# Kernel optimization log

Measured on AMD Instinct MI355X. Metric: run time of the kernel, lower is better.

Reference implementation:

```python
import jax, jax.numpy as jnp
import numpy as np

B, N, IN_DIM, OUT_DIM, K = 64, 256, 512, 512, 8
DK = OUT_DIM // K  # per-kernel feature dim


def setup_inputs() -> dict:
    key = jax.random.key(0)
    k1, k2, k3, k4 = jax.random.split(key, 4)
    node_feats = jax.random.normal(k1, (B, N, IN_DIM), dtype=jnp.float32)
    adj = jax.random.uniform(k2, (B, K, N, N), dtype=jnp.float32)
    weight = jax.random.normal(k3, (IN_DIM, OUT_DIM), dtype=jnp.float32) * (1.0 / np.sqrt(IN_DIM))
    bias = jax.random.normal(k4, (OUT_DIM,), dtype=jnp.float32) * 0.01
    return {"node_feats": node_feats, "adj": adj, "weight": weight, "bias": bias}


def reference(node_feats, adj, weight, bias):
    # kernel linear + ReLU: (b, n, out_dim)
    h = jax.nn.relu(jnp.einsum('bni,io->bno', node_feats, weight) + bias)
    # split into kernel slots: (b, n, k, dk)
    h = h.reshape(B, N, K, DK)
    # graph.aggregate: per-kernel dense message passing over adjacency
    # out[b,n,k,d] = sum_m adj[b,k,n,m] * h[b,m,k,d]
    agg = jnp.einsum('bknm,bmkd->bnkd', adj, h)
    return agg.reshape(B, N, OUT_DIM)
```

## Files before the change

kernel.cpp:

```cpp
#include <hip/hip_runtime.h>
#include <hip/hip_bf16.h>


typedef __attribute__((ext_vector_type(8))) short short8;
typedef __attribute__((ext_vector_type(4))) float floatx4;

__device__ __forceinline__ unsigned short f2bf(float f) {
    union { float f; unsigned u; } v; v.f = f;
    unsigned r = v.u + 0x7FFFu + ((v.u >> 16) & 1u);
    return (unsigned short)(r >> 16);
}

__device__ __forceinline__ unsigned pk2bf(float a, float b) {
    union { __hip_bfloat162 h; unsigned u; } cv;
    cv.h = __float22bfloat162_rn(make_float2(a, b));
    return cv.u;
}

__global__ __launch_bounds__(256) void wfrag_kernel(const float* __restrict__ W,
                                                    unsigned short* __restrict__ Wf) {
    __shared__ unsigned short t[32 * 66];
    const int blk = blockIdx.x;
    const int k0 = (blk & 15) * 32;
    const int o0 = (blk >> 4) * 64;
    const int tid = threadIdx.x;
#pragma unroll
    for (int j = 0; j < 8; ++j) {
        int idx = tid + j * 256;
        int oc = idx & 63, kr = idx >> 6;
        t[kr * 66 + oc] = f2bf(W[(size_t)(k0 + kr) * 512 + o0 + oc]);
    }
    __syncthreads();
#pragma unroll
    for (int j = 0; j < 8; ++j) {
        int idx = tid + j * 256;
        int kk = idx & 31, dr = idx >> 5;
        Wf[(size_t)blk * 2048 + dr * 32 + kk] = t[kk * 66 + dr];
    }
}

__global__ __launch_bounds__(256, 5) void lin_kernel(
    const float* __restrict__ X, const unsigned short* __restrict__ Wf,
    const float* __restrict__ bias, unsigned short* __restrict__ hF) {
    __shared__ unsigned short xt[2][128 * 40];

    const int W_ = (blockIdx.x & 7) * 128 + (blockIdx.x >> 3);
    const int mh = W_ & 1;
    const int ks = (W_ >> 1) & 7;
    const int b  = W_ >> 4;

    const int tid = threadIdx.x;
    const int lane = tid & 63, w = tid >> 6;
    const int lrow = lane & 15, quad = lane >> 4;

    const float* xsrc = X + (size_t)b * 131072
                          + (size_t)(mh * 128 + (tid >> 1)) * 512 + (tid & 1) * 16;
    const int xw = (tid >> 1) * 40 + (tid & 1) * 16;

    const unsigned short* wfp = Wf + (size_t)ks * 32768 + lrow * 32 + quad * 8;

    float bv[4];
#pragma unroll
    for (int dt = 0; dt < 4; ++dt) bv[dt] = bias[ks * 64 + dt * 16 + lrow];

    floatx4 acc[2][4];
    const floatx4 fzero = {0.f, 0.f, 0.f, 0.f};
#pragma unroll
    for (int g = 0; g < 2; ++g)
#pragma unroll
        for (int j = 0; j < 4; ++j) acc[g][j] = fzero;

    float4 r[4];
#define LLOAD(kb) do {                                                  \
        r[0] = *(const float4*)(xsrc + (kb) * 32);                      \
        r[1] = *(const float4*)(xsrc + (kb) * 32 + 4);                  \
        r[2] = *(const float4*)(xsrc + (kb) * 32 + 8);                  \
        r[3] = *(const float4*)(xsrc + (kb) * 32 + 12);                 \
    } while (0)
#define LWRITE(buf) do {                                                \
        union { short8 s; unsigned u[4]; } t0_, t1_;                    \
        t0_.u[0] = pk2bf(r[0].x, r[0].y); t0_.u[1] = pk2bf(r[0].z, r[0].w); \
        t0_.u[2] = pk2bf(r[1].x, r[1].y); t0_.u[3] = pk2bf(r[1].z, r[1].w); \
        t1_.u[0] = pk2bf(r[2].x, r[2].y); t1_.u[1] = pk2bf(r[2].z, r[2].w); \
        t1_.u[2] = pk2bf(r[3].x, r[3].y); t1_.u[3] = pk2bf(r[3].z, r[3].w); \
        *(short8*)(xt[buf] + xw) = t0_.s;                               \
        *(short8*)(xt[buf] + xw + 8) = t1_.s;                           \
    } while (0)

    LLOAD(0);
    LWRITE(0);
    LLOAD(1);
    __syncthreads();

#pragma unroll
    for (int kb = 0; kb < 16; ++kb) {
        const int buf = kb & 1;
        if (kb < 15) {
            LWRITE(buf ^ 1);
            if (kb < 14) LLOAD(kb + 2);
        }
        short8 a0 = *(const short8*)(xt[buf] + (w * 32 + lrow) * 40 + quad * 8);
        short8 a1 = *(const short8*)(xt[buf] + (w * 32 + 16 + lrow) * 40 + quad * 8);
#pragma unroll
        for (int dt = 0; dt < 4; ++dt) {
            short8 wfr = *(const short8*)(wfp + kb * 2048 + dt * 512);
            acc[0][dt] = __builtin_amdgcn_mfma_f32_16x16x32_bf16(a0, wfr, acc[0][dt], 0, 0, 0);
            acc[1][dt] = __builtin_amdgcn_mfma_f32_16x16x32_bf16(a1, wfr, acc[1][dt], 0, 0, 0);
        }
        if (kb < 15) __syncthreads();
    }
#undef LLOAD
#undef LWRITE

    unsigned short* hs = hF + (size_t)(b * 8 + ks) * 16384 + (size_t)(mh * 4 + w) * 2048;
#pragma unroll
    for (int g = 0; g < 2; ++g) {
#pragma unroll
        for (int dt = 0; dt < 4; ++dt) {
            floatx4 c = acc[g][dt];
            uint2 pv;
            pv.x = pk2bf(fmaxf(c.x + bv[dt], 0.f), fmaxf(c.y + bv[dt], 0.f));
            pv.y = pk2bf(fmaxf(c.z + bv[dt], 0.f), fmaxf(c.w + bv[dt], 0.f));
            *(uint2*)(hs + dt * 512 + lrow * 32 + g * 16 + quad * 4) = pv;
        }
    }
}

__global__ __launch_bounds__(256, 5) void agg_kernel(
    const unsigned short* __restrict__ hF, const float* __restrict__ adj,
    float* __restrict__ out) {
    __shared__ unsigned short at[2][128 * 40];

    const int W_ = (blockIdx.x & 7) * 128 + (blockIdx.x >> 3);
    const int nt = W_ & 1;
    const int ks = (W_ >> 1) & 7;
    const int b  = W_ >> 4;

    const int tid = threadIdx.x;
    const int lane = tid & 63, w = tid >> 6;
    const int lrow = lane & 15, quad = lane >> 4;

    const float* asrc = adj + (size_t)(b * 8 + ks) * 65536
                            + (size_t)(nt * 128 + (tid >> 1)) * 256 + (tid & 1) * 16;
    const int aw = (tid >> 1) * 40 + (tid & 1) * 16;

    const unsigned short* hfp = hF + (size_t)(b * 8 + ks) * 16384 + lrow * 32 + quad * 8;

    floatx4 acc[2][4];
    const floatx4 fzero = {0.f, 0.f, 0.f, 0.f};
#pragma unroll
    for (int g = 0; g < 2; ++g)
#pragma unroll
        for (int j = 0; j < 4; ++j) acc[g][j] = fzero;

    float4 r[4];
#define ALOAD(mt) do {                                                  \
        r[0] = *(const float4*)(asrc + (mt) * 32);                      \
        r[1] = *(const float4*)(asrc + (mt) * 32 + 4);                  \
        r[2] = *(const float4*)(asrc + (mt) * 32 + 8);                  \
        r[3] = *(const float4*)(asrc + (mt) * 32 + 12);                 \
    } while (0)
#define AWRITE(buf) do {                                                \
        union { short8 s; unsigned u[4]; } t0_, t1_;                    \
        t0_.u[0] = pk2bf(r[0].x, r[0].y); t0_.u[1] = pk2bf(r[0].z, r[0].w); \
        t0_.u[2] = pk2bf(r[1].x, r[1].y); t0_.u[3] = pk2bf(r[1].z, r[1].w); \
        t1_.u[0] = pk2bf(r[2].x, r[2].y); t1_.u[1] = pk2bf(r[2].z, r[2].w); \
        t1_.u[2] = pk2bf(r[3].x, r[3].y); t1_.u[3] = pk2bf(r[3].z, r[3].w); \
        *(short8*)(at[buf] + aw) = t0_.s;                               \
        *(short8*)(at[buf] + aw + 8) = t1_.s;                           \
    } while (0)

    ALOAD(0);
    AWRITE(0);
    ALOAD(1);
    __syncthreads();

#pragma unroll
    for (int mt = 0; mt < 8; ++mt) {
        const int buf = mt & 1;
        if (mt < 7) {
            AWRITE(buf ^ 1);
            if (mt < 6) ALOAD(mt + 2);
        }
        short8 a0 = *(const short8*)(at[buf] + (w * 32 + lrow) * 40 + quad * 8);
        short8 a1 = *(const short8*)(at[buf] + (w * 32 + 16 + lrow) * 40 + quad * 8);
#pragma unroll
        for (int dt = 0; dt < 4; ++dt) {
            short8 hfr = *(const short8*)(hfp + mt * 2048 + dt * 512);
            acc[0][dt] = __builtin_amdgcn_mfma_f32_16x16x32_bf16(a0, hfr, acc[0][dt], 0, 0, 0);
            acc[1][dt] = __builtin_amdgcn_mfma_f32_16x16x32_bf16(a1, hfr, acc[1][dt], 0, 0, 0);
        }
        if (mt < 7) __syncthreads();
    }
#undef ALOAD
#undef AWRITE

#pragma unroll
    for (int g = 0; g < 2; ++g) {
        const int n0 = nt * 128 + w * 32 + g * 16 + quad * 4;
        float* dst = out + ((size_t)b * 256 + n0) * 512 + ks * 64 + lrow;
#pragma unroll
        for (int dt = 0; dt < 4; ++dt) {
            float* p = dst + dt * 16;
            p[0 * 512] = acc[g][dt].x;
            p[1 * 512] = acc[g][dt].y;
            p[2 * 512] = acc[g][dt].z;
            p[3 * 512] = acc[g][dt].w;
        }
    }
}

extern "C" void kernel_launch(void* const* d_in, const int* in_sizes, int n_in,
                              void* d_out, int out_size, void* d_ws, size_t ws_size,
                              hipStream_t stream) {
    const float* X    = (const float*)d_in[0];
    const float* adj  = (const float*)d_in[1];
    const float* W    = (const float*)d_in[2];
    const float* bias = (const float*)d_in[3];
    float* out = (float*)d_out;

    unsigned short* Wf = (unsigned short*)d_ws;
    unsigned short* hF = Wf + 512 * 512;

    wfrag_kernel<<<128, 256, 0, stream>>>(W, Wf);
    lin_kernel<<<1024, 256, 0, stream>>>(X, Wf, bias, hF);
    agg_kernel<<<1024, 256, 0, stream>>>(hF, adj, out);
}
```

Before: 271.5 us.

## Single-buffer LDS with register double-buffered prefetch and lighter barriers

Both GEMM kernels drop the double-buffered LDS tile for a single buffer and keep two register sets of fp32 global loads, prefetching two tiles ahead. Weight and h fragments for the next step are also prefetched into registers. The __syncthreads calls become explicit lgkmcnt waits plus s_barrier wrapped in sched_barrier, and launch bounds drop from 5 to 4 waves per SIMD. This is meant to hide global-load latency better, at the cost of two barriers per iteration, higher register pressure and lower occupancy.

```diff
diff --git a/kernel.cpp b/kernel.cpp
--- a/kernel.cpp
+++ b/kernel.cpp
@@ -15,6 +15,13 @@
     union { __hip_bfloat162 h; unsigned u; } cv;
     cv.h = __float22bfloat162_rn(make_float2(a, b));
     return cv.u;
+}
+
+__device__ __forceinline__ void lds_barrier() {
+    __builtin_amdgcn_sched_barrier(0);
+    asm volatile("s_waitcnt lgkmcnt(0)" ::: "memory");
+    __builtin_amdgcn_s_barrier();
+    __builtin_amdgcn_sched_barrier(0);
 }
 
 __global__ __launch_bounds__(256) void wfrag_kernel(const float* __restrict__ W,
@@ -39,10 +46,10 @@
     }
 }
 
-__global__ __launch_bounds__(256, 5) void lin_kernel(
+__global__ __launch_bounds__(256, 4) void lin_kernel(
     const float* __restrict__ X, const unsigned short* __restrict__ Wf,
     const float* __restrict__ bias, unsigned short* __restrict__ hF) {
-    __shared__ unsigned short xt[2][128 * 40];
+    __shared__ unsigned short xt[128 * 40];
 
     const int W_ = (blockIdx.x & 7) * 128 + (blockIdx.x >> 3);
     const int mh = W_ & 1;
@@ -70,44 +77,50 @@
 #pragma unroll
         for (int j = 0; j < 4; ++j) acc[g][j] = fzero;
 
-    float4 r[4];
-#define LLOAD(kb) do {                                                  \
+    float4 ra[4], rb[4];
+    short8 wc[4], wn[4];
+
+#define LLOAD(r, kb) do {                                               \
         r[0] = *(const float4*)(xsrc + (kb) * 32);                      \
         r[1] = *(const float4*)(xsrc + (kb) * 32 + 4);                  \
         r[2] = *(const float4*)(xsrc + (kb) * 32 + 8);                  \
         r[3] = *(const float4*)(xsrc + (kb) * 32 + 12);                 \
     } while (0)
-#define LWRITE(buf) do {                                                \
+#define LWRITE(r) do {                                                  \
         union { short8 s; unsigned u[4]; } t0_, t1_;                    \
         t0_.u[0] = pk2bf(r[0].x, r[0].y); t0_.u[1] = pk2bf(r[0].z, r[0].w); \
         t0_.u[2] = pk2bf(r[1].x, r[1].y); t0_.u[3] = pk2bf(r[1].z, r[1].w); \
         t1_.u[0] = pk2bf(r[2].x, r[2].y); t1_.u[1] = pk2bf(r[2].z, r[2].w); \
         t1_.u[2] = pk2bf(r[3].x, r[3].y); t1_.u[3] = pk2bf(r[3].z, r[3].w); \
-        *(short8*)(xt[buf] + xw) = t0_.s;                               \
-        *(short8*)(xt[buf] + xw + 8) = t1_.s;                           \
-    } while (0)
-
-    LLOAD(0);
-    LWRITE(0);
-    LLOAD(1);
-    __syncthreads();
+        *(short8*)(xt + xw) = t0_.s;                                    \
+        *(short8*)(xt + xw + 8) = t1_.s;                                \
+    } while (0)
+
+    LLOAD(ra, 0);
+    LLOAD(rb, 1);
+#pragma unroll
+    for (int dt = 0; dt < 4; ++dt) wc[dt] = *(const short8*)(wfp + dt * 512);
 
 #pragma unroll
     for (int kb = 0; kb < 16; ++kb) {
-        const int buf = kb & 1;
+        if (kb > 0) lds_barrier();
+        if (kb & 1) { LWRITE(rb); if (kb < 14) LLOAD(rb, kb + 2); }
+        else        { LWRITE(ra); if (kb < 14) LLOAD(ra, kb + 2); }
         if (kb < 15) {
-            LWRITE(buf ^ 1);
-            if (kb < 14) LLOAD(kb + 2);
-        }
-        short8 a0 = *(const short8*)(xt[buf] + (w * 32 + lrow) * 40 + quad * 8);
-        short8 a1 = *(const short8*)(xt[buf] + (w * 32 + 16 + lrow) * 40 + quad * 8);
-#pragma unroll
-        for (int dt = 0; dt < 4; ++dt) {
-            short8 wfr = *(const short8*)(wfp + kb * 2048 + dt * 512);
-            acc[0][dt] = __builtin_amdgcn_mfma_f32_16x16x32_bf16(a0, wfr, acc[0][dt], 0, 0, 0);
-            acc[1][dt] = __builtin_amdgcn_mfma_f32_16x16x32_bf16(a1, wfr, acc[1][dt], 0, 0, 0);
-        }
-        if (kb < 15) __syncthreads();
+#pragma unroll
+            for (int dt = 0; dt < 4; ++dt)
+                wn[dt] = *(const short8*)(wfp + (kb + 1) * 2048 + dt * 512);
+        }
+        lds_barrier();
+        short8 a0 = *(const short8*)(xt + (w * 32 + lrow) * 40 + quad * 8);
+        short8 a1 = *(const short8*)(xt + (w * 32 + 16 + lrow) * 40 + quad * 8);
+#pragma unroll
+        for (int dt = 0; dt < 4; ++dt) {
+            acc[0][dt] = __builtin_amdgcn_mfma_f32_16x16x32_bf16(a0, wc[dt], acc[0][dt], 0, 0, 0);
+            acc[1][dt] = __builtin_amdgcn_mfma_f32_16x16x32_bf16(a1, wc[dt], acc[1][dt], 0, 0, 0);
+        }
+#pragma unroll
+        for (int dt = 0; dt < 4; ++dt) wc[dt] = wn[dt];
     }
 #undef LLOAD
 #undef LWRITE
@@ -126,10 +139,10 @@
     }
 }
 
-__global__ __launch_bounds__(256, 5) void agg_kernel(
+__global__ __launch_bounds__(256, 4) void agg_kernel(
     const unsigned short* __restrict__ hF, const float* __restrict__ adj,
     float* __restrict__ out) {
-    __shared__ unsigned short at[2][128 * 40];
+    __shared__ unsigned short at[128 * 40];
 
     const int W_ = (blockIdx.x & 7) * 128 + (blockIdx.x >> 3);
     const int nt = W_ & 1;
@@ -153,44 +166,50 @@
 #pragma unroll
         for (int j = 0; j < 4; ++j) acc[g][j] = fzero;
 
-    float4 r[4];
-#define ALOAD(mt) do {                                                  \
+    float4 ra[4], rb[4];
+    short8 hc[4], hn[4];
+
+#define ALOAD(r, mt) do {                                               \
         r[0] = *(const float4*)(asrc + (mt) * 32);                      \
         r[1] = *(const float4*)(asrc + (mt) * 32 + 4);                  \
         r[2] = *(const float4*)(asrc + (mt) * 32 + 8);                  \
         r[3] = *(const float4*)(asrc + (mt) * 32 + 12);                 \
     } while (0)
-#define AWRITE(buf) do {                                                \
+#define AWRITE(r) do {                                                  \
         union { short8 s; unsigned u[4]; } t0_, t1_;                    \
         t0_.u[0] = pk2bf(r[0].x, r[0].y); t0_.u[1] = pk2bf(r[0].z, r[0].w); \
         t0_.u[2] = pk2bf(r[1].x, r[1].y); t0_.u[3] = pk2bf(r[1].z, r[1].w); \
         t1_.u[0] = pk2bf(r[2].x, r[2].y); t1_.u[1] = pk2bf(r[2].z, r[2].w); \
         t1_.u[2] = pk2bf(r[3].x, r[3].y); t1_.u[3] = pk2bf(r[3].z, r[3].w); \
-        *(short8*)(at[buf] + aw) = t0_.s;                               \
-        *(short8*)(at[buf] + aw + 8) = t1_.s;                           \
-    } while (0)
-
-    ALOAD(0);
-    AWRITE(0);
-    ALOAD(1);
-    __syncthreads();
+        *(short8*)(at + aw) = t0_.s;                                    \
+        *(short8*)(at + aw + 8) = t1_.s;                                \
+    } while (0)
+
+    ALOAD(ra, 0);
+    ALOAD(rb, 1);
+#pragma unroll
+    for (int dt = 0; dt < 4; ++dt) hc[dt] = *(const short8*)(hfp + dt * 512);
 
 #pragma unroll
     for (int mt = 0; mt < 8; ++mt) {
-        const int buf = mt & 1;
+        if (mt > 0) lds_barrier();
+        if (mt & 1) { AWRITE(rb); if (mt < 6) ALOAD(rb, mt + 2); }
+        else        { AWRITE(ra); if (mt < 6) ALOAD(ra, mt + 2); }
         if (mt < 7) {
-            AWRITE(buf ^ 1);
-            if (mt < 6) ALOAD(mt + 2);
-        }
-        short8 a0 = *(const short8*)(at[buf] + (w * 32 + lrow) * 40 + quad * 8);
-        short8 a1 = *(const short8*)(at[buf] + (w * 32 + 16 + lrow) * 40 + quad * 8);
-#pragma unroll
-        for (int dt = 0; dt < 4; ++dt) {
-            short8 hfr = *(const short8*)(hfp + mt * 2048 + dt * 512);
-            acc[0][dt] = __builtin_amdgcn_mfma_f32_16x16x32_bf16(a0, hfr, acc[0][dt], 0, 0, 0);
-            acc[1][dt] = __builtin_amdgcn_mfma_f32_16x16x32_bf16(a1, hfr, acc[1][dt], 0, 0, 0);
-        }
-        if (mt < 7) __syncthreads();
+#pragma unroll
+            for (int dt = 0; dt < 4; ++dt)
+                hn[dt] = *(const short8*)(hfp + (mt + 1) * 2048 + dt * 512);
+        }
+        lds_barrier();
+        short8 a0 = *(const short8*)(at + (w * 32 + lrow) * 40 + quad * 8);
+        short8 a1 = *(const short8*)(at + (w * 32 + 16 + lrow) * 40 + quad * 8);
+#pragma unroll
+        for (int dt = 0; dt < 4; ++dt) {
+            acc[0][dt] = __builtin_amdgcn_mfma_f32_16x16x32_bf16(a0, hc[dt], acc[0][dt], 0, 0, 0);
+            acc[1][dt] = __builtin_amdgcn_mfma_f32_16x16x32_bf16(a1, hc[dt], acc[1][dt], 0, 0, 0);
+        }
+#pragma unroll
+        for (int dt = 0; dt < 4; ++dt) hc[dt] = hn[dt];
     }
 #undef ALOAD
 #undef AWRITE
```

After: 262.8 us. -3.2%, faster.
